# Kernel tuning notes

Measured on AMD Instinct MI355X. Metric: run time of the kernel, lower is better.

## Reference

```python
import jax, jax.numpy as jnp
import numpy as np

H = 1024   # longformer-large hidden size
D = 256    # transformer d_model / args.hidden_dim
Q = 100    # num_queries / num_slots
N = 1024   # document length (unpadded tokens)
L = 30     # args.max_span_length
WD = 20    # span width embedding dim
S = N * L - L * (L - 1) // 2  # 30285 candidate spans


def _ln(x, g, b, eps=1e-5):
    m = jnp.mean(x, -1, keepdims=True)
    v = jnp.mean((x - m) ** 2, -1, keepdims=True)
    return (x - m) * jax.lax.rsqrt(v + eps) * g + b


def setup_inputs():
    ks = jax.random.split(jax.random.key(0), 16)
    # deterministic span enumeration: triu(0) & tril(L-1) mention mask, row-major
    idx = np.arange(N)
    m = (idx[None, :] >= idx[:, None]) & (idx[None, :] < idx[:, None] + L)
    ss, ee = np.nonzero(m)
    assert ss.shape[0] == S
    r = lambda i, shape, s=0.02: jax.random.normal(ks[i], shape, jnp.float32) * s
    z = lambda *shape: jnp.zeros(shape, jnp.float32)
    o = lambda *shape: jnp.ones(shape, jnp.float32)
    return dict(
        encoded_doc=jax.random.normal(ks[0], (1, N, H), jnp.float32),
        span_starts=jnp.asarray(ss, jnp.int32),
        span_ends=jnp.asarray(ee, jnp.int32),
        w_word_attn=r(1, (H, 1)), b_word_attn=z(1),
        span_width_embed=r(2, (L, WD)),
        w_span_proj=r(3, (3 * H + WD, D)), b_span_proj=z(D),
        slots_query=r(4, (Q, D)),
        wq=r(5, (D, D)), bq=z(D),
        wk=r(6, (D, D)), bk=z(D),
        wv=r(7, (D, D)), bv=z(D),
        w_ih=r(8, (3 * D, D)), w_hh=r(9, (3 * D, D)), b_ih=z(3 * D), b_hh=z(3 * D),
        w_mlp1=r(10, (D, 2 * D)), b_mlp1=z(2 * D),
        w_mlp2=r(11, (2 * D, D)), b_mlp2=z(D),
        g_in=o(D), beta_in=z(D),
        g_sl=o(D), beta_sl=z(D),
        g_ff=o(D), beta_ff=z(D),
    )


def reference(encoded_doc, span_starts, span_ends, w_word_attn, b_word_attn,
              span_width_embed, w_span_proj, b_span_proj, slots_query,
              wq, bq, wk, bk, wv, bv, w_ih, w_hh, b_ih, b_hh,
              w_mlp1, b_mlp1, w_mlp2, b_mlp2,
              g_in, beta_in, g_sl, beta_sl, g_ff, beta_ff):
    doc = encoded_doc[0]                                   # [N, H]
    # --- get_span_emb ---
    start_emb = doc[span_starts]                           # [S, H]
    end_emb = doc[span_ends]                               # [S, H]
    width_idx = jnp.minimum(1 + span_ends - span_starts, L) - 1
    width_emb = span_width_embed[width_idx]                # [S, WD]
    word_attn = (doc @ w_word_attn)[:, 0] + b_word_attn[0] # [N]
    pos = jnp.arange(N)
    smask = (pos[None, :] >= span_starts[:, None]) & (pos[None, :] <= span_ends[:, None])
    scores = jnp.where(smask, word_attn[None, :], -jnp.inf)  # log(mask)+attn
    head = jax.nn.softmax(scores, axis=-1) @ doc           # [S, H]
    span_emb = jnp.concatenate([start_emb, end_emb, width_emb, head], -1)[None]  # [1,S,3H+WD]
    x = span_emb @ w_span_proj + b_span_proj               # [1, S, D]
    # --- slot attention ---
    inputs = _ln(x, g_in, beta_in)
    k = inputs @ wk + bk
    v = inputs @ wv + bv
    scale = D ** -0.5
    eps = 1e-8
    slots = slots_query[None]                              # [1, Q, D]
    for _ in range(3):
        slots_prev = slots
        q = _ln(slots, g_sl, beta_sl) @ wq + bq
        dots = jnp.einsum('bid,bjd->bij', q, k) * scale    # [1, Q, S]
        attn = jax.nn.softmax(dots, axis=1) + eps          # softmax over slots!
        attn = attn / jnp.sum(attn, -1, keepdims=True)
        updates = jnp.einsum('bjd,bij->bid', v, attn)      # [1, Q, D]
        # torch GRUCell
        xg = updates.reshape(-1, D)
        h = slots_prev.reshape(-1, D)
        gi = xg @ w_ih.T + b_ih
        gh = h @ w_hh.T + b_hh
        ir, iz, inn = jnp.split(gi, 3, -1)
        hr, hz, hn = jnp.split(gh, 3, -1)
        rg = jax.nn.sigmoid(ir + hr)
        zg = jax.nn.sigmoid(iz + hz)
        ng = jnp.tanh(inn + rg * hn)
        slots = ((1.0 - zg) * ng + zg * h).reshape(1, -1, D)
        ff = _ln(slots, g_ff, beta_ff)
        slots = slots + jax.nn.relu(ff @ w_mlp1 + b_mlp1) @ w_mlp2 + b_mlp2
    q = _ln(slots, g_sl, beta_sl) @ wq + bq
    dots = jnp.einsum('bid,bjd->bij', q, k) * scale
    coref_logits = jnp.minimum(jax.nn.softmax(dots, axis=1) + eps, 1.0)  # [1, Q, S]
    return coref_logits, inputs
```

## Files before the change

kernel.cpp:

```cpp
#include <hip/hip_runtime.h>

#define S_TOT 30285
#define SPAD  30720
#define EPS_S 3.0285e-4f

typedef __attribute__((ext_vector_type(8))) short bf16x8;
typedef __attribute__((ext_vector_type(4))) float f32x4;

__device__ __forceinline__ unsigned short f2bf(float f) {
  unsigned u = __float_as_uint(f);
  u += 0x7FFFu + ((u >> 16) & 1u);
  return (unsigned short)(u >> 16);
}
__device__ __forceinline__ float bf2f(unsigned short h) {
  return __uint_as_float(((unsigned)h) << 16);
}
__device__ __forceinline__ float allred_sum(float v) {
#pragma unroll
  for (int o = 32; o > 0; o >>= 1) v += __shfl_xor(v, o, 64);
  return v;
}

__global__ void k_prep(const float* __restrict__ doc, const float* __restrict__ w_wa,
                       const float* __restrict__ b_wa, const float* __restrict__ wemb,
                       const float* __restrict__ wsp, const float* __restrict__ wk,
                       const float* __restrict__ wv, const float* __restrict__ wq,
                       const float* __restrict__ w1, const float* __restrict__ w2,
                       const float* __restrict__ wih, const float* __restrict__ whh,
                       const float* __restrict__ slots_q, float* __restrict__ wa,
                       float* __restrict__ Wd, unsigned short* __restrict__ docb,
                       unsigned short* __restrict__ wihb, unsigned short* __restrict__ whhb,
                       unsigned short* __restrict__ wspT, unsigned short* __restrict__ wkT,
                       unsigned short* __restrict__ wvT, unsigned short* __restrict__ wqT,
                       unsigned short* __restrict__ w1T, unsigned short* __restrict__ w2T,
                       float* __restrict__ slots, float* __restrict__ zeroF,
                       unsigned short* __restrict__ inbpad) {
  __shared__ float shf[1056];
  int b = blockIdx.x, t = threadIdx.x;
  if (b < 1024) {
    float s = 0.f;
    for (int h = t; h < 1024; h += 256) s += doc[b * 1024 + h] * w_wa[h];
    shf[t] = s;
    __syncthreads();
    for (int o = 128; o; o >>= 1) {
      if (t < o) shf[t] += shf[t + o];
      __syncthreads();
    }
    if (t == 0) wa[b] = shf[0] + b_wa[0];
  } else if (b < 1054) {
    int w = b - 1024;
    float s = 0.f;
    for (int j = 0; j < 20; j++) s += wemb[w * 20 + j] * wsp[(2048 + j) * 256 + t];
    Wd[w * 256 + t] = s;
  } else if (b < 6686) {
    int b2 = b - 1054;
    if (b2 < 4096) { int i = b2 * 256 + t; docb[i] = f2bf(doc[i]); }
    else if (b2 < 4864) { int i = (b2 - 4096) * 256 + t; wihb[i] = f2bf(wih[i]); }
    else { int i = (b2 - 4864) * 256 + t; whhb[i] = f2bf(whh[i]); }
  } else if (b < 7902) {
    int bb = b - 6686;
    const float* src; unsigned short* dst; int R, C, tid;
    if (bb < 768) {
      int sec = bb >> 8; tid = bb & 255;
      src = wsp + (sec == 0 ? 0 : (sec == 1 ? 1024 * 256 : 2068 * 256));
      dst = wspT + (size_t)sec * 256 * 1024; R = 1024; C = 256;
    } else if (bb < 832) { src = wk; dst = wkT; R = 256; C = 256; tid = bb - 768; }
    else if (bb < 896) { src = wv; dst = wvT; R = 256; C = 256; tid = bb - 832; }
    else if (bb < 960) { src = wq; dst = wqT; R = 256; C = 256; tid = bb - 896; }
    else if (bb < 1088) { src = w1; dst = w1T; R = 256; C = 512; tid = bb - 960; }
    else { src = w2; dst = w2T; R = 512; C = 256; tid = bb - 1088; }
    int cw = C >> 5;
    int c0 = (tid % cw) * 32, r0 = (tid / cw) * 32;
#pragma unroll
    for (int i = 0; i < 4; i++) {
      int e = i * 256 + t, rr = e >> 5, cc = e & 31;
      shf[rr * 33 + cc] = src[(size_t)(r0 + rr) * C + c0 + cc];
    }
    __syncthreads();
#pragma unroll
    for (int i = 0; i < 4; i++) {
      int e = i * 256 + t, cc = e >> 5, rr = e & 31;
      dst[(size_t)(c0 + cc) * R + r0 + rr] = f2bf(shf[rr * 33 + cc]);
    }
  } else if (b < 7909) {
    int r0 = (b - 7902) * 16;
    for (int rr = 0; rr < 16; rr++) {
      int row = r0 + rr;
      slots[row * 256 + t] = (row < 100) ? slots_q[row * 256 + t] : 0.f;
    }
  } else if (b < 7994) {
    int i4 = (b - 7909) * 256 + t;
    if (i4 < 21664) ((float4*)zeroF)[i4] = (float4){0.f, 0.f, 0.f, 0.f};
  } else {
    int i = (b - 7994) * 256 + t;
    if (i < 13920) ((uint4*)inbpad)[i] = (uint4){0u, 0u, 0u, 0u};
  }
}

__global__ __launch_bounds__(256) void k_abc_mfma(const unsigned short* __restrict__ docb,
                                                  const unsigned short* __restrict__ wspT,
                                                  float* __restrict__ A, float* __restrict__ B,
                                                  float* __restrict__ C) {
  int rt = blockIdx.x, sec = blockIdx.y;
  float* out = sec == 0 ? A : (sec == 1 ? B : C);
  const unsigned short* wt = wspT + (size_t)sec * 256 * 1024;
  __shared__ unsigned short lds[64 * 256];
  int t = threadIdx.x, w = t >> 6, l = t & 63, lr = l & 15, lh = l >> 4;
  f32x4 acc[4][4];
#pragma unroll
  for (int m = 0; m < 4; m++)
#pragma unroll
    for (int n = 0; n < 4; n++) acc[m][n] = (f32x4){0.f, 0.f, 0.f, 0.f};
  for (int kt = 0; kt < 4; kt++) {
    __syncthreads();
#pragma unroll
    for (int it = 0; it < 8; it++) {
      int e = it * 256 + t, row = e >> 5, c16 = e & 31;
      int ba = ((row * 512) + c16 * 16) ^ ((row & 7) << 4);
      *(uint4*)((char*)lds + ba) =
          *(const uint4*)(docb + (size_t)(rt * 64 + row) * 1024 + kt * 256 + c16 * 8);
    }
    __syncthreads();
    for (int kk = 0; kk < 8; kk++) {
      bf16x8 afr[4];
#pragma unroll
      for (int m = 0; m < 4; m++) {
        int row = m * 16 + lr;
        int ba = ((row * 512) + kk * 64 + lh * 16) ^ ((row & 7) << 4);
        afr[m] = *(bf16x8*)((char*)lds + ba);
      }
#pragma unroll
      for (int n = 0; n < 4; n++) {
        bf16x8 b8 = *(const bf16x8*)(wt + (size_t)(w * 64 + n * 16 + lr) * 1024 + kt * 256 +
                                     kk * 32 + lh * 8);
#pragma unroll
        for (int m = 0; m < 4; m++)
          acc[m][n] = __builtin_amdgcn_mfma_f32_16x16x32_bf16(afr[m], b8, acc[m][n], 0, 0, 0);
      }
    }
  }
#pragma unroll
  for (int n = 0; n < 4; n++) {
    int col = w * 64 + n * 16 + lr;
#pragma unroll
    for (int m = 0; m < 4; m++)
#pragma unroll
      for (int r = 0; r < 4; r++)
        out[(size_t)(rt * 64 + m * 16 + lh * 4 + r) * 256 + col] = acc[m][n][r];
  }
}

__global__ void k_spans_ln(const float* __restrict__ wa, const float* __restrict__ A,
                           const float* __restrict__ B, const float* __restrict__ C,
                           const float* __restrict__ Wd, const float* __restrict__ bias,
                           const float* __restrict__ g_in, const float* __restrict__ be_in,
                           float* __restrict__ xin, unsigned short* __restrict__ inb) {
  int ss = blockIdx.x, t = threadIdx.x;
  int w = t >> 6, lane = t & 63;
  int nsp = min(30, 1024 - ss);
  int base = (ss < 995) ? ss * 30 : 29850 + 435 - ((1024 - ss) * (1025 - ss)) / 2;
  __shared__ float C_l[30 * 256];
  __shared__ float wa_l[30];
  for (int e = t; e < nsp * 256; e += 256)
    C_l[e] = C[(ss + (e >> 8)) * 256 + (e & 255)];
  if (t < nsp) wa_l[t] = wa[ss + t];
  __syncthreads();
  int c0 = lane * 4;
  float4 aS = *(const float4*)(A + ss * 256 + c0);
  float4 bi = *(const float4*)(bias + c0);
  float a0 = aS.x + bi.x, a1 = aS.y + bi.y, a2 = aS.z + bi.z, a3 = aS.w + bi.w;
  float4 gg = *(const float4*)(g_in + c0);
  float4 bb = *(const float4*)(be_in + c0);
  float m = -3.4e38f, Z = 0.f;
  float W0 = 0.f, W1 = 0.f, W2 = 0.f, W3 = 0.f;
  int pos = 0;
  for (int sp = w; sp < nsp; sp += 4) {
    for (; pos <= sp; ++pos) {
      float as_ = wa_l[pos];
      float mn = fmaxf(m, as_);
      float corr = __expf(m - mn);
      float e = __expf(as_ - mn);
      Z = Z * corr + e;
      float4 cc = *(const float4*)(C_l + pos * 256 + c0);
      W0 = W0 * corr + e * cc.x;
      W1 = W1 * corr + e * cc.y;
      W2 = W2 * corr + e * cc.z;
      W3 = W3 * corr + e * cc.w;
      m = mn;
    }
    float invZ = 1.f / Z;
    float4 Bv = *(const float4*)(B + (size_t)(ss + sp) * 256 + c0);
    float4 wd = *(const float4*)(Wd + sp * 256 + c0);
    float v0 = a0 + Bv.x + wd.x + W0 * invZ;
    float v1 = a1 + Bv.y + wd.y + W1 * invZ;
    float v2 = a2 + Bv.z + wd.z + W2 * invZ;
    float v3 = a3 + Bv.w + wd.w + W3 * invZ;
    float s = allred_sum(v0 + v1 + v2 + v3);
    float mean = s * (1.f / 256.f);
    float d0 = v0 - mean, d1 = v1 - mean, d2 = v2 - mean, d3 = v3 - mean;
    float q = allred_sum(d0 * d0 + d1 * d1 + d2 * d2 + d3 * d3);
    float rstd = rsqrtf(q * (1.f / 256.f) + 1e-5f);
    float o0 = d0 * rstd * gg.x + bb.x;
    float o1 = d1 * rstd * gg.y + bb.y;
    float o2 = d2 * rstd * gg.z + bb.z;
    float o3 = d3 * rstd * gg.w + bb.w;
    size_t r = (size_t)(base + sp) * 256 + c0;
    *(float4*)(xin + r) = (float4){o0, o1, o2, o3};
    ushort4 u4;
    u4.x = f2bf(o0); u4.y = f2bf(o1); u4.z = f2bf(o2); u4.w = f2bf(o3);
    *(ushort4*)(inb + r) = u4;
  }
}

__global__ __launch_bounds__(256) void k_kv_mfma(const unsigned short* __restrict__ inb,
                                                 const unsigned short* __restrict__ wkT,
                                                 const unsigned short* __restrict__ wvT,
                                                 const float* __restrict__ bk,
                                                 const float* __restrict__ bv,
                                                 unsigned short* __restrict__ kb,
                                                 unsigned short* __restrict__ vT,
                                                 float* __restrict__ vsum) {
  int j0 = blockIdx.x * 64;
  int t = threadIdx.x, w = t >> 6, l = t & 63, lr = l & 15, lh = l >> 4;
  __shared__ unsigned short lds[64 * 256];
#pragma unroll
  for (int it = 0; it < 8; it++) {
    int e = it * 256 + t, row = e >> 5, c16 = e & 31;
    int ba = ((row * 512) + c16 * 16) ^ ((row & 7) << 4);
    *(uint4*)((char*)lds + ba) = *(const uint4*)(inb + (size_t)(j0 + row) * 256 + c16 * 8);
  }
  __syncthreads();
  f32x4 ak[4][4], av[4][4];
#pragma unroll
  for (int m = 0; m < 4; m++)
#pragma unroll
    for (int n = 0; n < 4; n++) {
      ak[m][n] = (f32x4){0.f, 0.f, 0.f, 0.f};
      av[m][n] = (f32x4){0.f, 0.f, 0.f, 0.f};
    }
  for (int kk = 0; kk < 8; kk++) {
    bf16x8 afr[4];
#pragma unroll
    for (int m = 0; m < 4; m++) {
      int row = m * 16 + lr;
      int ba = ((row * 512) + kk * 64 + lh * 16) ^ ((row & 7) << 4);
      afr[m] = *(bf16x8*)((char*)lds + ba);
    }
#pragma unroll
    for (int n = 0; n < 4; n++) {
      int col = w * 64 + n * 16 + lr;
      bf16x8 bk8 = *(const bf16x8*)(wkT + (size_t)col * 256 + kk * 32 + lh * 8);
      bf16x8 bv8 = *(const bf16x8*)(wvT + (size_t)col * 256 + kk * 32 + lh * 8);
#pragma unroll
      for (int m = 0; m < 4; m++) {
        ak[m][n] = __builtin_amdgcn_mfma_f32_16x16x32_bf16(afr[m], bk8, ak[m][n], 0, 0, 0);
        av[m][n] = __builtin_amdgcn_mfma_f32_16x16x32_bf16(afr[m], bv8, av[m][n], 0, 0, 0);
      }
    }
  }
#pragma unroll
  for (int n = 0; n < 4; n++) {
    int col = w * 64 + n * 16 + lr;
    float bks = bk[col], bvs = bv[col];
    float cs = 0.f;
#pragma unroll
    for (int m = 0; m < 4; m++)
#pragma unroll
      for (int r = 0; r < 4; r++) {
        int row = j0 + m * 16 + lh * 4 + r;
        float kvv = ak[m][n][r] + bks;
        float vvv = av[m][n][r] + bvs;
        kb[(size_t)row * 256 + col] = f2bf(kvv);
        vT[(size_t)col * SPAD + row] = f2bf(vvv);
        if (row < S_TOT) cs += vvv;
      }
    cs += __shfl_xor(cs, 16, 64);
    cs += __shfl_xor(cs, 32, 64);
    if (lh == 0) atomicAdd(&vsum[col], cs);
  }
}

__global__ void k_qln0(const float* __restrict__ slots, const float* __restrict__ g_sl,
                       const float* __restrict__ be_sl, const unsigned short* __restrict__ wqT,
                       const float* __restrict__ bq, unsigned short* __restrict__ qbf) {
  int i = blockIdx.x, t = threadIdx.x;
  if (i >= 100) { qbf[i * 256 + t] = 0; return; }
  __shared__ float ln_l[256];
  __shared__ float red[8];
  int wave = t >> 6, lane = t & 63;
  float v = slots[i * 256 + t];
  float s = allred_sum(v);
  if (lane == 0) red[wave] = s;
  __syncthreads();
  float mean = (red[0] + red[1] + red[2] + red[3]) * (1.f / 256.f);
  float dv = v - mean;
  float s2 = allred_sum(dv * dv);
  if (lane == 0) red[4 + wave] = s2;
  __syncthreads();
  float var = (red[4] + red[5] + red[6] + red[7]) * (1.f / 256.f);
  ln_l[t] = dv * rsqrtf(var + 1e-5f) * g_sl[t] + be_sl[t];
  __syncthreads();
  float q = bq[t];
  size_t c = (size_t)t * 256;
  for (int d = 0; d < 256; d += 8) {
    bf16x8 a = *(const bf16x8*)(wqT + c + d);
#pragma unroll
    for (int e = 0; e < 8; e++) q += bf2f((unsigned short)a[e]) * ln_l[d + e];
  }
  qbf[i * 256 + t] = f2bf(q);
}

__global__ __launch_bounds__(256) void k_dots_f(const unsigned short* __restrict__ kb,
                                                const unsigned short* __restrict__ qb,
                                                unsigned short* __restrict__ pT,
                                                float* __restrict__ rowsum,
                                                float* __restrict__ coref, int final_, int S_) {
  int j0 = blockIdx.x * 64;
  int t = threadIdx.x, w = t >> 6, l = t & 63, lr = l & 15, lh = l >> 4;
  f32x4 acc[7];
#pragma unroll
  for (int n = 0; n < 7; n++) acc[n] = (f32x4){0.f, 0.f, 0.f, 0.f};
  const unsigned short* arow = kb + (size_t)(j0 + w * 16 + lr) * 256;
  for (int kk = 0; kk < 8; kk++) {
    bf16x8 a8 = *(const bf16x8*)(arow + kk * 32 + lh * 8);
#pragma unroll
    for (int n = 0; n < 7; n++) {
      bf16x8 b8 = *(const bf16x8*)(qb + (size_t)(n * 16 + lr) * 256 + kk * 32 + lh * 8);
      acc[n] = __builtin_amdgcn_mfma_f32_16x16x32_bf16(a8, b8, acc[n], 0, 0, 0);
    }
  }
  __shared__ float dt[64][117];
#pragma unroll
  for (int n = 0; n < 7; n++)
#pragma unroll
    for (int r = 0; r < 4; r++) dt[w * 16 + lh * 4 + r][n * 16 + lr] = acc[n][r] * 0.0625f;
  __syncthreads();
  int jj = t >> 2, q4 = t & 3;
  float mx = -3.4e38f;
#pragma unroll
  for (int i = 0; i < 25; i++) mx = fmaxf(mx, dt[jj][q4 * 25 + i]);
  mx = fmaxf(mx, __shfl_xor(mx, 1, 64));
  mx = fmaxf(mx, __shfl_xor(mx, 2, 64));
  float sm = 0.f;
#pragma unroll
  for (int i = 0; i < 25; i++) {
    float e = __expf(dt[jj][q4 * 25 + i] - mx);
    dt[jj][q4 * 25 + i] = e;
    sm += e;
  }
  sm += __shfl_xor(sm, 1, 64);
  sm += __shfl_xor(sm, 2, 64);
  float inv = 1.f / sm;
#pragma unroll
  for (int i = 0; i < 25; i++) dt[jj][q4 * 25 + i] *= inv;
  __syncthreads();
  if (!final_) {
    for (int e = t; e < 112 * 64; e += 256) {
      int i = e >> 6, j2 = e & 63;
      float pv = (i < 100 && (j0 + j2) < S_) ? dt[j2][i] : 0.f;
      pT[(size_t)i * SPAD + j0 + j2] = f2bf(pv);
    }
    int nv = S_ - j0;
    if (nv > 64) nv = 64;
    if (t < 100) {
      float s = 0.f;
      for (int j2 = 0; j2 < nv; j2++) s += dt[j2][t];
      atomicAdd(rowsum + t, s);
    }
  } else {
    for (int e = t; e < 100 * 64; e += 256) {
      int i = e >> 6, j2 = e & 63;
      if ((j0 + j2) < S_) coref[(size_t)i * S_ + j0 + j2] = fminf(dt[j2][i] + 1e-8f, 1.0f);
    }
  }
}

__global__ __launch_bounds__(256) void k_upd_mfma(const unsigned short* __restrict__ pT,
                                                  const unsigned short* __restrict__ vT,
                                                  float* __restrict__ uraw) {
  int kc = blockIdx.x, ny = blockIdx.y;
  int t = threadIdx.x, w = t >> 6, l = t & 63, lr = l & 15, lh = l >> 4;
  int k0 = kc * 320;
  int c0 = ny * 128 + w * 32;
  f32x4 acc[7][2];
#pragma unroll
  for (int m = 0; m < 7; m++) {
    acc[m][0] = (f32x4){0.f, 0.f, 0.f, 0.f};
    acc[m][1] = (f32x4){0.f, 0.f, 0.f, 0.f};
  }
  for (int ks = 0; ks < 10; ks++) {
    int kof = k0 + ks * 32 + lh * 8;
    bf16x8 b0 = *(const bf16x8*)(vT + (size_t)(c0 + lr) * SPAD + kof);
    bf16x8 b1 = *(const bf16x8*)(vT + (size_t)(c0 + 16 + lr) * SPAD + kof);
#pragma unroll
    for (int m = 0; m < 7; m++) {
      bf16x8 a8 = *(const bf16x8*)(pT + (size_t)(m * 16 + lr) * SPAD + kof);
      acc[m][0] = __builtin_amdgcn_mfma_f32_16x16x32_bf16(a8, b0, acc[m][0], 0, 0, 0);
      acc[m][1] = __builtin_amdgcn_mfma_f32_16x16x32_bf16(a8, b1, acc[m][1], 0, 0, 0);
    }
  }
#pragma unroll
  for (int m = 0; m < 7; m++)
#pragma unroll
    for (int n = 0; n < 2; n++)
#pragma unroll
      for (int r = 0; r < 4; r++) {
        int i = m * 16 + lh * 4 + r;
        if (i < 100) atomicAdd(&uraw[i * 256 + c0 + n * 16 + lr], acc[m][n][r]);
      }
}


#define WBUF_EL 8448

__device__ __forceinline__ void gemv_g256(const unsigned short* __restrict__ W, int nchunks,
                                          const float* __restrict__ xl, float* __restrict__ outp,
                                          unsigned short* __restrict__ wbuf, int t) {
  __syncthreads();
  int s = t & 7, r = t >> 3;
  float xseg[32];
#pragma unroll
  for (int k = 0; k < 8; k++) *(float4*)&xseg[k * 4] = *(const float4*)&xl[s * 32 + k * 4];
  bf16x8 pf[4];
#pragma unroll
  for (int q = 0; q < 4; q++) pf[q] = *(const bf16x8*)(W + (size_t)(q * 256 + t) * 8);
  for (int n = 0; n < nchunks; n++) {
    unsigned short* buf = wbuf + (n & 1) * WBUF_EL;
#pragma unroll
    for (int q = 0; q < 4; q++) {
      int idx = q * 256 + t;
      *(bf16x8*)(buf + (idx >> 5) * 264 + (idx & 31) * 8) = pf[q];
    }
    if (n + 1 < nchunks) {
      const unsigned short* src = W + (size_t)(n + 1) * 8192;
#pragma unroll
      for (int q = 0; q < 4; q++) pf[q] = *(const bf16x8*)(src + (size_t)(q * 256 + t) * 8);
    }
    __syncthreads();
    const unsigned short* row = wbuf + (n & 1) * WBUF_EL + r * 264 + s * 32;
    float acc = 0.f;
#pragma unroll
    for (int k8 = 0; k8 < 4; k8++) {
      bf16x8 a = *(const bf16x8*)(row + k8 * 8);
#pragma unroll
      for (int e = 0; e < 8; e++) acc += bf2f((unsigned short)a[e]) * xseg[k8 * 8 + e];
    }
    acc += __shfl_xor(acc, 1, 64);
    acc += __shfl_xor(acc, 2, 64);
    acc += __shfl_xor(acc, 4, 64);
    if (s == 0) outp[n * 32 + r] = acc;
  }
  __syncthreads();
}

__device__ __forceinline__ void gemv_g512(const unsigned short* __restrict__ W, int nchunks,
                                          const float* __restrict__ xl, float* __restrict__ outp,
                                          unsigned short* __restrict__ wbuf, int t) {
  __syncthreads();
  int s = t & 15, r = t >> 4;
  float xseg[32];
#pragma unroll
  for (int k = 0; k < 8; k++) *(float4*)&xseg[k * 4] = *(const float4*)&xl[s * 32 + k * 4];
  bf16x8 pf[4];
#pragma unroll
  for (int q = 0; q < 4; q++) pf[q] = *(const bf16x8*)(W + (size_t)(q * 256 + t) * 8);
  for (int n = 0; n < nchunks; n++) {
    unsigned short* buf = wbuf + (n & 1) * WBUF_EL;
#pragma unroll
    for (int q = 0; q < 4; q++) {
      int idx = q * 256 + t;
      *(bf16x8*)(buf + (idx >> 6) * 520 + (idx & 63) * 8) = pf[q];
    }
    if (n + 1 < nchunks) {
      const unsigned short* src = W + (size_t)(n + 1) * 8192;
#pragma unroll
      for (int q = 0; q < 4; q++) pf[q] = *(const bf16x8*)(src + (size_t)(q * 256 + t) * 8);
    }
    __syncthreads();
    const unsigned short* row = wbuf + (n & 1) * WBUF_EL + r * 520 + s * 32;
    float acc = 0.f;
#pragma unroll
    for (int k8 = 0; k8 < 4; k8++) {
      bf16x8 a = *(const bf16x8*)(row + k8 * 8);
#pragma unroll
      for (int e = 0; e < 8; e++) acc += bf2f((unsigned short)a[e]) * xseg[k8 * 8 + e];
    }
    acc += __shfl_xor(acc, 1, 64);
    acc += __shfl_xor(acc, 2, 64);
    acc += __shfl_xor(acc, 4, 64);
    acc += __shfl_xor(acc, 8, 64);
    if (s == 0) outp[n * 16 + r] = acc;
  }
  __syncthreads();
}

__global__ __launch_bounds__(256) void k_slot_tail(
    const float* __restrict__ uraw, const float* __restrict__ vsum,
    const float* __restrict__ rs, float* __restrict__ slots,
    const unsigned short* __restrict__ wihb, const unsigned short* __restrict__ whhb,
    const float* __restrict__ b_ih, const float* __restrict__ b_hh,
    const unsigned short* __restrict__ w1T, const float* __restrict__ b1,
    const unsigned short* __restrict__ w2T, const float* __restrict__ b2,
    const float* __restrict__ g_ff, const float* __restrict__ be_ff,
    const float* __restrict__ g_sl, const float* __restrict__ be_sl,
    const unsigned short* __restrict__ wqT, const float* __restrict__ bq,
    unsigned short* __restrict__ qbf) {
  int i = blockIdx.x, t = threadIdx.x;
  __shared__ float u_l[256], h_l[256], shid[512];
  __shared__ float gacc[1536];
  __shared__ unsigned short wbuf[2 * WBUF_EL];
  __shared__ float red[8];
  int wave = t >> 6, lane = t & 63;
  float u = (uraw[i * 256 + t] + 1e-8f * vsum[t]) / (rs[i] + EPS_S);
  float h = slots[i * 256 + t];
  u_l[t] = u;
  h_l[t] = h;
  gemv_g256(wihb, 24, u_l, gacc, wbuf, t);
  gemv_g256(whhb, 24, h_l, gacc + 768, wbuf, t);
  float gA0 = gacc[t] + b_ih[t];
  float gA1 = gacc[256 + t] + b_ih[t + 256];
  float gA2 = gacc[512 + t] + b_ih[t + 512];
  float gB0 = gacc[768 + t] + b_hh[t];
  float gB1 = gacc[1024 + t] + b_hh[t + 256];
  float gB2 = gacc[1280 + t] + b_hh[t + 512];
  float rg = 1.f / (1.f + __expf(-(gA0 + gB0)));
  float zg = 1.f / (1.f + __expf(-(gA1 + gB1)));
  float ng = tanhf(gA2 + rg * gB2);
  float ns_ = (1.f - zg) * ng + zg * h;
  float s = allred_sum(ns_);
  if (lane == 0) red[wave] = s;
  __syncthreads();
  float mean = (red[0] + red[1] + red[2] + red[3]) * (1.f / 256.f);
  float dv = ns_ - mean;
  float s2 = allred_sum(dv * dv);
  if (lane == 0) red[4 + wave] = s2;
  __syncthreads();
  float var = (red[4] + red[5] + red[6] + red[7]) * (1.f / 256.f);
  u_l[t] = dv * rsqrtf(var + 1e-5f) * g_ff[t] + be_ff[t];
  gemv_g256(w1T, 16, u_l, gacc, wbuf, t);
  shid[t] = fmaxf(gacc[t] + b1[t], 0.f);
  shid[t + 256] = fmaxf(gacc[t + 256] + b1[t + 256], 0.f);
  gemv_g512(w2T, 16, shid, gacc, wbuf, t);
  float o = ns_ + b2[t] + gacc[t];
  slots[i * 256 + t] = o;
  float s3 = allred_sum(o);
  if (lane == 0) red[wave] = s3;
  __syncthreads();
  float mean2 = (red[0] + red[1] + red[2] + red[3]) * (1.f / 256.f);
  float dv2 = o - mean2;
  float s4 = allred_sum(dv2 * dv2);
  if (lane == 0) red[4 + wave] = s4;
  __syncthreads();
  float var2 = (red[4] + red[5] + red[6] + red[7]) * (1.f / 256.f);
  h_l[t] = dv2 * rsqrtf(var2 + 1e-5f) * g_sl[t] + be_sl[t];
  gemv_g256(wqT, 8, h_l, gacc, wbuf, t);
  qbf[i * 256 + t] = f2bf(bq[t] + gacc[t]);
}

extern "C" void kernel_launch(void* const* d_in, const int* in_sizes, int n_in,
                              void* d_out, int out_size, void* d_ws, size_t ws_size,
                              hipStream_t stream) {
  const float* doc = (const float*)d_in[0];
  const float* w_wa = (const float*)d_in[3];
  const float* b_wa = (const float*)d_in[4];
  const float* wemb = (const float*)d_in[5];
  const float* wsp = (const float*)d_in[6];
  const float* bsp = (const float*)d_in[7];
  const float* slots_q = (const float*)d_in[8];
  const float* wq = (const float*)d_in[9];
  const float* bq = (const float*)d_in[10];
  const float* wk = (const float*)d_in[11];
  const float* bk = (const float*)d_in[12];
  const float* wv = (const float*)d_in[13];
  const float* bv = (const float*)d_in[14];
  const float* w_ih = (const float*)d_in[15];
  const float* w_hh = (const float*)d_in[16];
  const float* b_ih = (const float*)d_in[17];
  const float* b_hh = (const float*)d_in[18];
  const float* w1 = (const float*)d_in[19];
  const float* b1 = (const float*)d_in[20];
  const float* w2 = (const float*)d_in[21];
  const float* b2 = (const float*)d_in[22];
  const float* g_in = (const float*)d_in[23];
  const float* be_in = (const float*)d_in[24];
  const float* g_sl = (const float*)d_in[25];
  const float* be_sl = (const float*)d_in[26];
  const float* g_ff = (const float*)d_in[27];
  const float* be_ff = (const float*)d_in[28];

  const int S = S_TOT;
  float* out = (float*)d_out;
  float* coref = out;
  float* xin = out + 100 * S;

  float* ws = (float*)d_ws;
  float* wa = ws;
  float* Wd = wa + 1024;
  float* A = Wd + 7680;
  float* Bm = A + 262144;
  float* Cm = Bm + 262144;
  float* vsum = Cm + 262144;
  float* rowsum = vsum + 256;
  float* uraw = rowsum + 384;
  float* slots = uraw + 86016;
  unsigned short* ub = (unsigned short*)(slots + 28672);
  unsigned short* inb = ub;
  unsigned short* kbuf = inb + (size_t)SPAD * 256;
  unsigned short* vT = kbuf + (size_t)SPAD * 256;
  unsigned short* pT = vT + (size_t)SPAD * 256;
  unsigned short* qbf = pT + (size_t)112 * SPAD;
  unsigned short* docb = qbf + 112 * 256;
  unsigned short* wspT = docb + 1024 * 1024;
  unsigned short* wkT = wspT + 768 * 1024;
  unsigned short* wvT = wkT + 256 * 256;
  unsigned short* wqT = wvT + 256 * 256;
  unsigned short* wihb = wqT + 256 * 256;
  unsigned short* whhb = wihb + 768 * 256;
  unsigned short* w1T = whhb + 768 * 256;
  unsigned short* w2T = w1T + 512 * 256;

  k_prep<<<8049, 256, 0, stream>>>(doc, w_wa, b_wa, wemb, wsp, wk, wv, wq, w1, w2,
                                   w_ih, w_hh, slots_q, wa, Wd, docb, wihb, whhb, wspT,
                                   wkT, wvT, wqT, w1T, w2T, slots, vsum,
                                   inb + (size_t)S * 256);
  k_abc_mfma<<<dim3(16, 3), 256, 0, stream>>>(docb, wspT, A, Bm, Cm);
  k_spans_ln<<<1024, 256, 0, stream>>>(wa, A, Bm, Cm, Wd, bsp, g_in, be_in, xin, inb);
  k_kv_mfma<<<SPAD / 64, 256, 0, stream>>>(inb, wkT, wvT, bk, bv, kbuf, vT, vsum);
  k_qln0<<<112, 256, 0, stream>>>(slots, g_sl, be_sl, wqT, bq, qbf);

  for (int it = 0; it < 3; ++it) {
    float* rs_it = rowsum + it * 128;
    float* uraw_it = uraw + it * 28672;
    k_dots_f<<<SPAD / 64, 256, 0, stream>>>(kbuf, qbf, pT, rs_it, coref, 0, S);
    k_upd_mfma<<<dim3(96, 2), 256, 0, stream>>>(pT, vT, uraw_it);
    k_slot_tail<<<100, 256, 0, stream>>>(uraw_it, vsum, rs_it, slots, wihb, whhb,
                                         b_ih, b_hh, w1T, b1, w2T, b2, g_ff, be_ff,
                                         g_sl, be_sl, wqT, bq, qbf);
  }
  k_dots_f<<<SPAD / 64, 256, 0, stream>>>(kbuf, qbf, pT, rowsum, coref, 1, S);
}
```

Measured before the change: 408.2 us.

## Split GRU gate GEMVs into a batched MFMA kernel before slot tail

The GRU input and hidden gate projections move out of the per-slot tail kernel, where each of the 100 blocks streamed the full 768x256 weight matrices twice as GEMVs. A new k_gates kernel computes both projections for all slots at once as a 112x768 MFMA GEMM in bf16, writing gi/gh to workspace. The slot tail then reads those results, so the weights are read once per iteration rather than once per slot. The cost is an extra kernel launch per iteration, a global round trip for the gates, and only 24 blocks in the new kernel.

```diff
diff --git a/kernel.cpp b/kernel.cpp
--- a/kernel.cpp
+++ b/kernel.cpp
@@ -410,6 +410,66 @@
       }
 }
 
+__global__ __launch_bounds__(256) void k_gates(
+    const float* __restrict__ uraw, const float* __restrict__ vsum,
+    const float* __restrict__ rs, const float* __restrict__ slots,
+    const unsigned short* __restrict__ wihb, const unsigned short* __restrict__ whhb,
+    const float* __restrict__ b_ih, const float* __restrict__ b_hh,
+    float* __restrict__ gi, float* __restrict__ gh) {
+  int x = blockIdx.x, y = blockIdx.y;
+  const unsigned short* Wt = y ? whhb : wihb;
+  const float* bias = y ? b_hh : b_ih;
+  float* out = y ? gh : gi;
+  int t = threadIdx.x, w = t >> 6, l = t & 63, lr = l & 15, lh = l >> 4;
+  int col = x * 64 + w * 16 + lr;
+  f32x4 acc[7];
+#pragma unroll
+  for (int m = 0; m < 7; m++) acc[m] = (f32x4){0.f, 0.f, 0.f, 0.f};
+  for (int kk = 0; kk < 8; kk++) {
+    int d0 = kk * 32 + lh * 8;
+    bf16x8 b8 = *(const bf16x8*)(Wt + (size_t)col * 256 + d0);
+    if (y) {
+#pragma unroll
+      for (int m = 0; m < 7; m++) {
+        int row = m * 16 + lr;
+        float4 h0 = *(const float4*)(slots + row * 256 + d0);
+        float4 h1 = *(const float4*)(slots + row * 256 + d0 + 4);
+        bf16x8 a;
+        a[0] = (short)f2bf(h0.x); a[1] = (short)f2bf(h0.y);
+        a[2] = (short)f2bf(h0.z); a[3] = (short)f2bf(h0.w);
+        a[4] = (short)f2bf(h1.x); a[5] = (short)f2bf(h1.y);
+        a[6] = (short)f2bf(h1.z); a[7] = (short)f2bf(h1.w);
+        acc[m] = __builtin_amdgcn_mfma_f32_16x16x32_bf16(a, b8, acc[m], 0, 0, 0);
+      }
+    } else {
+      float4 vs0 = *(const float4*)(vsum + d0);
+      float4 vs1 = *(const float4*)(vsum + d0 + 4);
+#pragma unroll
+      for (int m = 0; m < 7; m++) {
+        int row = m * 16 + lr;
+        float inv = 1.f / (rs[row] + EPS_S);
+        float4 u0 = *(const float4*)(uraw + row * 256 + d0);
+        float4 u1 = *(const float4*)(uraw + row * 256 + d0 + 4);
+        bf16x8 a;
+        a[0] = (short)f2bf((u0.x + 1e-8f * vs0.x) * inv);
+        a[1] = (short)f2bf((u0.y + 1e-8f * vs0.y) * inv);
+        a[2] = (short)f2bf((u0.z + 1e-8f * vs0.z) * inv);
+        a[3] = (short)f2bf((u0.w + 1e-8f * vs0.w) * inv);
+        a[4] = (short)f2bf((u1.x + 1e-8f * vs1.x) * inv);
+        a[5] = (short)f2bf((u1.y + 1e-8f * vs1.y) * inv);
+        a[6] = (short)f2bf((u1.z + 1e-8f * vs1.z) * inv);
+        a[7] = (short)f2bf((u1.w + 1e-8f * vs1.w) * inv);
+        acc[m] = __builtin_amdgcn_mfma_f32_16x16x32_bf16(a, b8, acc[m], 0, 0, 0);
+      }
+    }
+  }
+  float bb = bias[col];
+#pragma unroll
+  for (int m = 0; m < 7; m++)
+#pragma unroll
+    for (int r = 0; r < 4; r++)
+      out[(size_t)(m * 16 + lh * 4 + r) * 768 + col] = acc[m][r] + bb;
+}
 
 #define WBUF_EL 8448
 
@@ -494,11 +554,9 @@
   __syncthreads();
 }
 
-__global__ __launch_bounds__(256) void k_slot_tail(
-    const float* __restrict__ uraw, const float* __restrict__ vsum,
-    const float* __restrict__ rs, float* __restrict__ slots,
-    const unsigned short* __restrict__ wihb, const unsigned short* __restrict__ whhb,
-    const float* __restrict__ b_ih, const float* __restrict__ b_hh,
+__global__ __launch_bounds__(256) void k_tail2(
+    const float* __restrict__ gi, const float* __restrict__ gh,
+    float* __restrict__ slots,
     const unsigned short* __restrict__ w1T, const float* __restrict__ b1,
     const unsigned short* __restrict__ w2T, const float* __restrict__ b2,
     const float* __restrict__ g_ff, const float* __restrict__ be_ff,
@@ -507,22 +565,13 @@
     unsigned short* __restrict__ qbf) {
   int i = blockIdx.x, t = threadIdx.x;
   __shared__ float u_l[256], h_l[256], shid[512];
-  __shared__ float gacc[1536];
+  __shared__ float gacc[512];
   __shared__ unsigned short wbuf[2 * WBUF_EL];
   __shared__ float red[8];
   int wave = t >> 6, lane = t & 63;
-  float u = (uraw[i * 256 + t] + 1e-8f * vsum[t]) / (rs[i] + EPS_S);
+  float gA0 = gi[i * 768 + t], gA1 = gi[i * 768 + 256 + t], gA2 = gi[i * 768 + 512 + t];
+  float gB0 = gh[i * 768 + t], gB1 = gh[i * 768 + 256 + t], gB2 = gh[i * 768 + 512 + t];
   float h = slots[i * 256 + t];
-  u_l[t] = u;
-  h_l[t] = h;
-  gemv_g256(wihb, 24, u_l, gacc, wbuf, t);
-  gemv_g256(whhb, 24, h_l, gacc + 768, wbuf, t);
-  float gA0 = gacc[t] + b_ih[t];
-  float gA1 = gacc[256 + t] + b_ih[t + 256];
-  float gA2 = gacc[512 + t] + b_ih[t + 512];
-  float gB0 = gacc[768 + t] + b_hh[t];
-  float gB1 = gacc[1024 + t] + b_hh[t + 256];
-  float gB2 = gacc[1280 + t] + b_hh[t + 512];
   float rg = 1.f / (1.f + __expf(-(gA0 + gB0)));
   float zg = 1.f / (1.f + __expf(-(gA1 + gB1)));
   float ng = tanhf(gA2 + rg * gB2);
@@ -603,7 +652,9 @@
   float* rowsum = vsum + 256;
   float* uraw = rowsum + 384;
   float* slots = uraw + 86016;
-  unsigned short* ub = (unsigned short*)(slots + 28672);
+  float* gi = slots + 28672;
+  float* gh = gi + 86016;
+  unsigned short* ub = (unsigned short*)(gh + 86016);
   unsigned short* inb = ub;
   unsigned short* kbuf = inb + (size_t)SPAD * 256;
   unsigned short* vT = kbuf + (size_t)SPAD * 256;
@@ -633,9 +684,10 @@
     float* uraw_it = uraw + it * 28672;
     k_dots_f<<<SPAD / 64, 256, 0, stream>>>(kbuf, qbf, pT, rs_it, coref, 0, S);
     k_upd_mfma<<<dim3(96, 2), 256, 0, stream>>>(pT, vT, uraw_it);
-    k_slot_tail<<<100, 256, 0, stream>>>(uraw_it, vsum, rs_it, slots, wihb, whhb,
-                                         b_ih, b_hh, w1T, b1, w2T, b2, g_ff, be_ff,
-                                         g_sl, be_sl, wqT, bq, qbf);
+    k_gates<<<dim3(12, 2), 256, 0, stream>>>(uraw_it, vsum, rs_it, slots, wihb, whhb,
+                                             b_ih, b_hh, gi, gh);
+    k_tail2<<<100, 256, 0, stream>>>(gi, gh, slots, w1T, b1, w2T, b2, g_ff, be_ff,
+                                     g_sl, be_sl, wqT, bq, qbf);
   }
   k_dots_f<<<SPAD / 64, 256, 0, stream>>>(kbuf, qbf, pT, rowsum, coref, 1, S);
 }
```

New measurement: 393.0 us, median of 2. 1.04x faster.
